# Optimization experiments

Hardware: AMD Instinct MI355X
Metric: run time of the kernel (lower is better)

## Reference

```python
import jax, jax.numpy as jnp
import numpy as np

LEN = 128
HIDDEN = 64
B, N = 256, 2048
LN_EPS = 1e-3  # keras LayerNormalization default epsilon
NEG_FILL = -1.0e9


def setup_inputs() -> dict:
    key = jax.random.key(0)
    k_in, k_m, k_w1, k_w2 = jax.random.split(key, 4)
    inputs = jax.random.normal(k_in, (B, N, LEN), dtype=jnp.float32)
    mask = jax.random.randint(k_m, (B, N), 0, 2) > 0
    # He-normal init for Dense kernels, zeros for biases (keras defaults)
    W1 = jax.random.normal(k_w1, (LEN, HIDDEN), dtype=jnp.float32) * np.sqrt(2.0 / LEN)
    b1 = jnp.zeros((HIDDEN,), dtype=jnp.float32)
    W2 = jax.random.normal(k_w2, (HIDDEN, LEN), dtype=jnp.float32) * np.sqrt(2.0 / HIDDEN)
    b2 = jnp.zeros((LEN,), dtype=jnp.float32)
    gamma = jnp.ones((LEN,), dtype=jnp.float32)
    beta = jnp.zeros((LEN,), dtype=jnp.float32)
    return {"inputs": inputs, "mask": mask, "W1": W1, "b1": b1,
            "W2": W2, "b2": b2, "gamma": gamma, "beta": beta}


def reference(inputs, mask, W1, b1, W2, b2, gamma, beta):
    # MLP: Dense -> Dense -> LayerNorm -> ReLU (weights shared over nodes)
    h = jnp.einsum('bnd,dh->bnh', inputs, W1) + b1          # [B,N,HIDDEN]
    h = jnp.einsum('bnh,hd->bnd', h, W2) + b2               # [B,N,LEN]
    mu = jnp.mean(h, axis=-1, keepdims=True)
    var = jnp.mean(jnp.square(h - mu), axis=-1, keepdims=True)
    h = (h - mu) * jax.lax.rsqrt(var + LN_EPS) * gamma + beta
    x = jax.nn.relu(h)                                      # [B,N,LEN]
    # masked fill (masked-out nodes set to large negative before max-pool)
    x = jnp.where(mask[:, :, None], x, NEG_FILL)
    # global max-pool over all N nodes, broadcast back, concat local+global
    x_pool = jnp.max(x, axis=1, keepdims=True)              # [B,1,LEN]
    x_tile = jnp.broadcast_to(x_pool, x.shape)              # [B,N,LEN]
    return jnp.concatenate([x, x_tile], axis=-1)            # [B,N,2*LEN]
```

## Files before the change

### kernel.cpp

```cpp
#include <hip/hip_runtime.h>
#include <hip/hip_bf16.h>

#define NEG_FILL -1.0e9f

using bf16x8 = __attribute__((ext_vector_type(8))) short;
using f32x4  = __attribute__((ext_vector_type(4))) float;

static __device__ __forceinline__ short f2bf(float f) {
    union { float f; unsigned u; } a; a.f = f;
    unsigned r = a.u + 0x7FFFu + ((a.u >> 16) & 1u);
    return (short)(r >> 16);
}

static __device__ __forceinline__ bf16x8 pack8(float4 a, float4 b) {
    union { __hip_bfloat162 h[4]; bf16x8 v; } u;
    u.h[0] = __float22bfloat162_rn({a.x, a.y});
    u.h[1] = __float22bfloat162_rn({a.z, a.w});
    u.h[2] = __float22bfloat162_rn({b.x, b.y});
    u.h[3] = __float22bfloat162_rn({b.z, b.w});
    return u.v;
}


__global__ __launch_bounds__(256) void k_prep(
    const float* __restrict__ W1, const float* __restrict__ b1,
    const float* __restrict__ W2, const float* __restrict__ b2,
    short* __restrict__ WT, float* __restrict__ beff, int* __restrict__ pool)
{
    int blk = blockIdx.x, tid = threadIdx.x;
    if (blk < 128) {
        pool[blk * 256 + tid] = __float_as_int(NEG_FILL);
        return;
    }
    if (blk < 192) {
        int e = (blk - 128) * 256 + tid;
        int n = e >> 7, k = e & 127;
        float s = 0.f;
        #pragma unroll 8
        for (int h = 0; h < 64; ++h) s = fmaf(W1[k * 64 + h], W2[h * 128 + n], s);
        WT[e] = f2bf(s);
    } else if (tid < 128) {
        float s = b2[tid];
        for (int h = 0; h < 64; ++h) s = fmaf(b1[h], W2[h * 128 + tid], s);
        beff[tid] = s;
    }
}

__global__ __launch_bounds__(256) void k_main(
    const float* __restrict__ X, const int* __restrict__ mask,
    const short* __restrict__ WT, const float* __restrict__ beff,
    const float* __restrict__ gamma, const float* __restrict__ beta,
    float* __restrict__ out, int* __restrict__ pool)
{
    __shared__ short Ws[128][136];
    __shared__ int pool_s[128];

    const int tid = threadIdx.x;
    const int rowbase = blockIdx.x * 256;

    if (tid < 128) pool_s[tid] = __float_as_int(NEG_FILL);

    #pragma unroll
    for (int i = 0; i < 8; ++i) {
        int g = tid + i * 256;
        int n = g >> 4, koff = (g & 15) * 8;
        *(bf16x8*)&Ws[n][koff] = *(const bf16x8*)(WT + g * 8);
    }

    const int wave = tid >> 6, lane = tid & 63;
    const int c = lane & 15, q = lane >> 4;

    float pm[8];
    #pragma unroll
    for (int t = 0; t < 8; ++t) pm[t] = NEG_FILL;

    __syncthreads();

    for (int grp = 0; grp < 4; ++grp) {
        const int rowloc = grp * 64 + wave * 16 + c;
        const float* __restrict__ xrow = X + (size_t)(rowbase + rowloc) * 128;

        f32x4 acc[8];
        const f32x4 zero = {0.f, 0.f, 0.f, 0.f};
        #pragma unroll
        for (int t = 0; t < 8; ++t) acc[t] = zero;

        #pragma unroll
        for (int kk = 0; kk < 4; ++kk) {
            float4 x0 = *(const float4*)(xrow + kk * 32 + q * 8);
            float4 x1 = *(const float4*)(xrow + kk * 32 + q * 8 + 4);
            bf16x8 a = pack8(x0, x1);
            #pragma unroll
            for (int t = 0; t < 8; ++t) {
                bf16x8 b = *(const bf16x8*)&Ws[t * 16 + c][kk * 32 + q * 8];
                acc[t] = __builtin_amdgcn_mfma_f32_16x16x32_bf16(a, b, acc[t], 0, 0, 0);
            }
        }

        float be[8], ga[8], bt[8];
        #pragma unroll
        for (int t = 0; t < 8; ++t) {
            int n = t * 16 + c;
            be[t] = beff[n]; ga[t] = gamma[n]; bt[t] = beta[n];
        }

        float v[8][4];
        #pragma unroll
        for (int t = 0; t < 8; ++t)
            #pragma unroll
            for (int r = 0; r < 4; ++r) v[t][r] = acc[t][r] + be[t];

        #pragma unroll
        for (int r = 0; r < 4; ++r) {
            float s = 0.f, s2 = 0.f;
            #pragma unroll
            for (int t = 0; t < 8; ++t) { s += v[t][r]; s2 = fmaf(v[t][r], v[t][r], s2); }
            #pragma unroll
            for (int m = 1; m < 16; m <<= 1) {
                s  += __shfl_xor(s,  m, 64);
                s2 += __shfl_xor(s2, m, 64);
            }
            float mu  = s * (1.f / 128.f);
            float var = s2 * (1.f / 128.f) - mu * mu;
            float rs  = rsqrtf(var + 1e-3f);
            int rg = rowbase + grp * 64 + wave * 16 + q * 4 + r;
            int mk = mask[rg];
            #pragma unroll
            for (int t = 0; t < 8; ++t) {
                float y = fmaf((v[t][r] - mu) * rs, ga[t], bt[t]);
                y = fmaxf(y, 0.f);
                y = mk ? y : NEG_FILL;
                v[t][r] = y;
                out[(size_t)rg * 256 + t * 16 + c] = y;
            }
        }

        #pragma unroll
        for (int t = 0; t < 8; ++t) {
            float g0 = fmaxf(fmaxf(v[t][0], v[t][1]), fmaxf(v[t][2], v[t][3]));
            pm[t] = fmaxf(pm[t], g0);
        }
    }

    #pragma unroll
    for (int t = 0; t < 8; ++t) {
        float p = pm[t];
        p = fmaxf(p, __shfl_xor(p, 16, 64));
        p = fmaxf(p, __shfl_xor(p, 32, 64));
        if (q == 0) atomicMax(&pool_s[t * 16 + c], __float_as_int(p));
    }
    __syncthreads();
    if (tid < 128) {
        int b = rowbase >> 11;
        atomicMax(&pool[b * 128 + tid], pool_s[tid]);
    }
}

__global__ __launch_bounds__(256) void k_bcast(
    const f32x4* __restrict__ pool4, f32x4* __restrict__ out4)
{
    unsigned base = blockIdx.x * 256 + threadIdx.x;
    #pragma unroll
    for (int i = 0; i < 16; ++i) {
        unsigned idx = base + (unsigned)i * (4096u * 256u);
        unsigned row = idx >> 5;
        unsigned c4  = idx & 31;
        unsigned b   = row >> 11;
        f32x4 pv = pool4[b * 32 + c4];
        __builtin_nontemporal_store(pv, &out4[(size_t)row * 64 + 32 + c4]);
    }
}

extern "C" void kernel_launch(void* const* d_in, const int* in_sizes, int n_in,
                              void* d_out, int out_size, void* d_ws, size_t ws_size,
                              hipStream_t stream)
{
    const float* X     = (const float*)d_in[0];
    const int*   mask  = (const int*)d_in[1];
    const float* W1    = (const float*)d_in[2];
    const float* b1    = (const float*)d_in[3];
    const float* W2    = (const float*)d_in[4];
    const float* b2    = (const float*)d_in[5];
    const float* gamma = (const float*)d_in[6];
    const float* beta  = (const float*)d_in[7];
    float* out = (float*)d_out;

    short* WT   = (short*)d_ws;
    float* beff = (float*)((char*)d_ws + 32768);
    int*   pool = (int*)((char*)d_ws + 33280);

    k_prep<<<193, 256, 0, stream>>>(W1, b1, W2, b2, WT, beff, pool);
    k_main<<<2048, 256, 0, stream>>>(X, mask, WT, beff, gamma, beta, out, pool);
    k_bcast<<<4096, 256, 0, stream>>>((const f32x4*)pool, (f32x4*)out);
}
```

Baseline: 765.7 us.

## Fuse max-pool broadcast into main kernel with one 1024-thread block per batch

```diff
diff --git a/kernel.cpp b/kernel.cpp
--- a/kernel.cpp
+++ b/kernel.cpp
@@ -25,15 +25,11 @@
 __global__ __launch_bounds__(256) void k_prep(
     const float* __restrict__ W1, const float* __restrict__ b1,
     const float* __restrict__ W2, const float* __restrict__ b2,
-    short* __restrict__ WT, float* __restrict__ beff, int* __restrict__ pool)
+    short* __restrict__ WT, float* __restrict__ beff)
 {
     int blk = blockIdx.x, tid = threadIdx.x;
-    if (blk < 128) {
-        pool[blk * 256 + tid] = __float_as_int(NEG_FILL);
-        return;
-    }
-    if (blk < 192) {
-        int e = (blk - 128) * 256 + tid;
+    if (blk < 64) {
+        int e = blk * 256 + tid;
         int n = e >> 7, k = e & 127;
         float s = 0.f;
         #pragma unroll 8
@@ -46,23 +42,24 @@
     }
 }
 
-__global__ __launch_bounds__(256) void k_main(
+__global__ __launch_bounds__(1024) void k_main(
     const float* __restrict__ X, const int* __restrict__ mask,
     const short* __restrict__ WT, const float* __restrict__ beff,
     const float* __restrict__ gamma, const float* __restrict__ beta,
-    float* __restrict__ out, int* __restrict__ pool)
+    float* __restrict__ out)
 {
     __shared__ short Ws[128][136];
-    __shared__ int pool_s[128];
+    __shared__ __align__(16) int pool_s[128];
 
-    const int tid = threadIdx.x;
-    const int rowbase = blockIdx.x * 256;
+    const int tid  = threadIdx.x;
+    const int bidx = blockIdx.x;
+    const size_t base_row = (size_t)bidx * 2048;
 
     if (tid < 128) pool_s[tid] = __float_as_int(NEG_FILL);
 
     #pragma unroll
-    for (int i = 0; i < 8; ++i) {
-        int g = tid + i * 256;
+    for (int i = 0; i < 2; ++i) {
+        int g = tid + i * 1024;
         int n = g >> 4, koff = (g & 15) * 8;
         *(bf16x8*)&Ws[n][koff] = *(const bf16x8*)(WT + g * 8);
     }
@@ -70,15 +67,32 @@
     const int wave = tid >> 6, lane = tid & 63;
     const int c = lane & 15, q = lane >> 4;
 
+    float be[8], ga[8], bt[8];
+    #pragma unroll
+    for (int t = 0; t < 8; ++t) {
+        int n = t * 16 + c;
+        be[t] = beff[n]; ga[t] = gamma[n]; bt[t] = beta[n];
+    }
+
     float pm[8];
     #pragma unroll
     for (int t = 0; t < 8; ++t) pm[t] = NEG_FILL;
 
     __syncthreads();
 
-    for (int grp = 0; grp < 4; ++grp) {
-        const int rowloc = grp * 64 + wave * 16 + c;
-        const float* __restrict__ xrow = X + (size_t)(rowbase + rowloc) * 128;
+    #pragma unroll 2
+    for (int it = 0; it < 8; ++it) {
+        const int row0 = it * 256 + wave * 16;
+        const float* __restrict__ xrow = X + (base_row + row0 + c) * 128;
+
+        bf16x8 afrag[4];
+        #pragma unroll
+        for (int kk = 0; kk < 4; ++kk) {
+            float4 x0 = *(const float4*)(xrow + kk * 32 + q * 8);
+            float4 x1 = *(const float4*)(xrow + kk * 32 + q * 8 + 4);
+            afrag[kk] = pack8(x0, x1);
+        }
+        const int4 mk4 = *(const int4*)(mask + base_row + row0 + q * 4);
 
         f32x4 acc[8];
         const f32x4 zero = {0.f, 0.f, 0.f, 0.f};
@@ -87,21 +101,11 @@
 
         #pragma unroll
         for (int kk = 0; kk < 4; ++kk) {
-            float4 x0 = *(const float4*)(xrow + kk * 32 + q * 8);
-            float4 x1 = *(const float4*)(xrow + kk * 32 + q * 8 + 4);
-            bf16x8 a = pack8(x0, x1);
             #pragma unroll
             for (int t = 0; t < 8; ++t) {
                 bf16x8 b = *(const bf16x8*)&Ws[t * 16 + c][kk * 32 + q * 8];
-                acc[t] = __builtin_amdgcn_mfma_f32_16x16x32_bf16(a, b, acc[t], 0, 0, 0);
+                acc[t] = __builtin_amdgcn_mfma_f32_16x16x32_bf16(afrag[kk], b, acc[t], 0, 0, 0);
             }
-        }
-
-        float be[8], ga[8], bt[8];
-        #pragma unroll
-        for (int t = 0; t < 8; ++t) {
-            int n = t * 16 + c;
-            be[t] = beff[n]; ga[t] = gamma[n]; bt[t] = beta[n];
         }
 
         float v[8][4];
@@ -110,6 +114,7 @@
             #pragma unroll
             for (int r = 0; r < 4; ++r) v[t][r] = acc[t][r] + be[t];
 
+        const int mks[4] = {mk4.x, mk4.y, mk4.z, mk4.w};
         #pragma unroll
         for (int r = 0; r < 4; ++r) {
             float s = 0.f, s2 = 0.f;
@@ -123,15 +128,15 @@
             float mu  = s * (1.f / 128.f);
             float var = s2 * (1.f / 128.f) - mu * mu;
             float rs  = rsqrtf(var + 1e-3f);
-            int rg = rowbase + grp * 64 + wave * 16 + q * 4 + r;
-            int mk = mask[rg];
+            size_t rg = base_row + row0 + q * 4 + r;
+            int mk = mks[r];
             #pragma unroll
             for (int t = 0; t < 8; ++t) {
                 float y = fmaf((v[t][r] - mu) * rs, ga[t], bt[t]);
                 y = fmaxf(y, 0.f);
                 y = mk ? y : NEG_FILL;
                 v[t][r] = y;
-                out[(size_t)rg * 256 + t * 16 + c] = y;
+                __builtin_nontemporal_store(y, &out[rg * 256 + t * 16 + c]);
             }
         }
 
@@ -150,24 +155,14 @@
         if (q == 0) atomicMax(&pool_s[t * 16 + c], __float_as_int(p));
     }
     __syncthreads();
-    if (tid < 128) {
-        int b = rowbase >> 11;
-        atomicMax(&pool[b * 128 + tid], pool_s[tid]);
-    }
-}
 
-__global__ __launch_bounds__(256) void k_bcast(
-    const f32x4* __restrict__ pool4, f32x4* __restrict__ out4)
-{
-    unsigned base = blockIdx.x * 256 + threadIdx.x;
-    #pragma unroll
-    for (int i = 0; i < 16; ++i) {
-        unsigned idx = base + (unsigned)i * (4096u * 256u);
-        unsigned row = idx >> 5;
-        unsigned c4  = idx & 31;
-        unsigned b   = row >> 11;
-        f32x4 pv = pool4[b * 32 + c4];
-        __builtin_nontemporal_store(pv, &out4[(size_t)row * 64 + 32 + c4]);
+    const f32x4 pv = ((const f32x4*)pool_s)[tid & 31];
+    f32x4* __restrict__ out4 = (f32x4*)out;
+    #pragma unroll 8
+    for (int i = 0; i < 64; ++i) {
+        int idx = tid + i * 1024;
+        size_t row = base_row + (idx >> 5);
+        __builtin_nontemporal_store(pv, &out4[row * 64 + 32 + (idx & 31)]);
     }
 }
 
@@ -187,9 +182,7 @@
 
     short* WT   = (short*)d_ws;
     float* beff = (float*)((char*)d_ws + 32768);
-    int*   pool = (int*)((char*)d_ws + 33280);
 
-    k_prep<<<193, 256, 0, stream>>>(W1, b1, W2, b2, WT, beff, pool);
-    k_main<<<2048, 256, 0, stream>>>(X, mask, WT, beff, gamma, beta, out, pool);
-    k_bcast<<<4096, 256, 0, stream>>>((const f32x4*)pool, (f32x4*)out);
+    k_prep<<<65, 256, 0, stream>>>(W1, b1, W2, b2, WT, beff);
+    k_main<<<256, 1024, 0, stream>>>(X, mask, WT, beff, gamma, beta, out);
 }
```

New measurement: 874.8 us. 1.14x slower.
